# Performance work log

Hardware: AMD Instinct MI355X
Metric: run time of the kernel (lower is better)

The kernel has to match this reference:

```python
import jax, jax.numpy as jnp
import numpy as np

B, N_LEAVES, HID, NCLS, VOCAB = 32, 512, 128, 2, 50257
N_NODES = 2 * N_LEAVES - 1  # complete binary tree, heap layout


def setup_inputs() -> dict:
    key = jax.random.key(0)
    ks = jax.random.split(key, 12)
    x = jax.random.randint(ks[0], (B, N_NODES), 0, VOCAB)
    cue = jax.random.randint(ks[1], (B, N_NODES), 0, NCLS)
    # word j sits at tree leaf node L-1+j
    word_index = jnp.tile(jnp.arange(N_LEAVES - 1, 2 * N_LEAVES - 1), (B, 1))
    # parent->child adjacency stored in adj[:, 1]
    A = np.zeros((2, N_NODES, N_NODES), dtype=bool)
    p = np.arange(N_LEAVES - 1)
    A[1, p, 2 * p + 1] = True
    A[1, p, 2 * p + 2] = True
    adj = jnp.asarray(np.broadcast_to(A, (B, 2, N_NODES, N_NODES)).copy())
    s = 0.05
    emb = jax.random.normal(ks[2], (VOCAB, HID - NCLS)) * s
    Wc = jax.random.normal(ks[3], (HID, 2 * HID)) * s
    bc = jax.random.normal(ks[4], (HID,)) * s
    Wd = jax.random.normal(ks[5], (2 * HID, 2 * HID)) * s
    bd = jax.random.normal(ks[6], (2 * HID,)) * s
    Wg = jax.random.normal(ks[7], (HID, HID)) * s
    bg = jax.random.normal(ks[8], (HID,)) * s
    Wcl = jax.random.normal(ks[9], (NCLS, 2 * HID)) * s
    bcl = jax.random.normal(ks[10], (NCLS,)) * s
    return dict(x=x, word_index=word_index, cue=cue, adj=adj, emb=emb,
                Wc=Wc, bc=bc, Wd=Wd, bd=bd, Wg=Wg, bg=bg, Wcl=Wcl, bcl=bcl)


def reference(x, word_index, cue, adj, emb, Wc, bc, Wd, bd, Wg, bg, Wcl, bcl):
    # adj encodes the same complete binary heap tree that is hardcoded below
    Bn, N = x.shape
    H = Wc.shape[0]
    C = bcl.shape[0]
    L = (N + 1) // 2
    depth = L.bit_length() - 1  # leaves live at level `depth`
    bidx = jnp.arange(Bn)[:, None]

    word_emb = emb[x]                                   # (B, N, H-C)
    cue_oh = jax.nn.one_hot(cue, C, dtype=word_emb.dtype)
    in_feats = jnp.concatenate([word_emb, cue_oh], -1)  # (B, N, H)
    sent = in_feats[bidx, word_index]                   # (B, L, H) leaf feats

    # ---- upward compose: level-batched bottom-up traversal ----
    h = jnp.zeros((Bn, N, H), in_feats.dtype).at[bidx, word_index].set(sent)
    for d in range(depth - 1, -1, -1):
        p = jnp.arange(2 ** d - 1, 2 ** (d + 1) - 1)
        ctx = jnp.concatenate([h[:, 2 * p + 1], h[:, 2 * p + 2]], -1)  # (B, 2^d, 2H)
        h = h.at[:, p].set(jnp.tanh(ctx @ Wc.T + bc))
    # upward_results never writes leaf rows -> leaves stay zero
    up = h.at[bidx, word_index].set(0.0)

    g_down = jax.nn.sigmoid(h[:, 0] @ Wg.T + bg)        # (B, H)

    # ---- downward decompose: level-batched top-down traversal ----
    down = jnp.zeros_like(h).at[:, 0].set(g_down)
    for d in range(depth):
        p = jnp.arange(2 ** d - 1, 2 ** (d + 1) - 1)
        ctx = jnp.concatenate([down[:, p], up[:, p]], -1)
        ch = jnp.tanh(ctx @ Wd.T + bd)                  # (B, 2^d, 2H)
        down = down.at[:, 2 * p + 1].set(ch[..., :H]).at[:, 2 * p + 2].set(ch[..., H:])

    tree = jnp.concatenate([down, up], -1)              # (B, N, 2H)
    scores = jax.nn.sigmoid(tree @ Wcl.T + bcl)
    return jax.nn.softmax(scores, -1)
```

## Files before the change

### kernel.cpp

```cpp
#include <hip/hip_runtime.h>
#include <hip/hip_fp16.h>


constexpr int NNODES = 1023;

typedef _Float16 h2 __attribute__((ext_vector_type(2)));

__device__ __forceinline__ float dot2(uint a, uint b, float c) {
  union { uint u; h2 h; } x, y;
  x.u = a; y.u = b;
  return __builtin_amdgcn_fdot2(x.h, y.h, c, false);
}

__device__ __forceinline__ uint f2h2(float a, float b) {
  return (uint)__half_as_ushort(__float2half_rn(a)) |
         ((uint)__half_as_ushort(__float2half_rn(b)) << 16);
}

__device__ __forceinline__ float2 h2f2(uint u) {
  union { uint u; h2 h; } c; c.u = u;
  return make_float2((float)c.h.x, (float)c.h.y);
}

__device__ __forceinline__ void load_wslice(const float* __restrict__ Wrow,
                                            int l16, int m, uint* wout) {
  const float4 f0 = *(const float4*)(Wrow + l16 * 8 + m * 128);
  const float4 f1 = *(const float4*)(Wrow + l16 * 8 + m * 128 + 4);
  wout[0] = f2h2(f0.x, f0.y);
  wout[1] = f2h2(f0.z, f0.w);
  wout[2] = f2h2(f1.x, f1.y);
  wout[3] = f2h2(f1.z, f1.w);
}

__device__ __forceinline__ float fold16(const float* a, int l) {
  float b[8];
#pragma unroll
  for (int u = 0; u < 8; ++u) {
    const float mine = (l & 1) ? a[2 * u + 1] : a[2 * u];
    const float oth  = (l & 1) ? a[2 * u]     : a[2 * u + 1];
    b[u] = mine + __shfl_xor(oth, 1);
  }
  float c[4];
#pragma unroll
  for (int u = 0; u < 4; ++u) {
    const float mine = (l & 2) ? b[2 * u + 1] : b[2 * u];
    const float oth  = (l & 2) ? b[2 * u]     : b[2 * u + 1];
    c[u] = mine + __shfl_xor(oth, 2);
  }
  float d[2];
#pragma unroll
  for (int u = 0; u < 2; ++u) {
    const float mine = (l & 4) ? c[2 * u + 1] : c[2 * u];
    const float oth  = (l & 4) ? c[2 * u]     : c[2 * u + 1];
    d[u] = mine + __shfl_xor(oth, 4);
  }
  const float mine = (l & 8) ? d[1] : d[0];
  const float oth  = (l & 8) ? d[0] : d[1];
  return mine + __shfl_xor(oth, 8);
}

__device__ __forceinline__ float fold8(const float* a, int l) {
  float b[4];
#pragma unroll
  for (int u = 0; u < 4; ++u) {
    const float mine = (l & 1) ? a[2 * u + 1] : a[2 * u];
    const float oth  = (l & 1) ? a[2 * u]     : a[2 * u + 1];
    b[u] = mine + __shfl_xor(oth, 1);
  }
  float c[2];
#pragma unroll
  for (int u = 0; u < 2; ++u) {
    const float mine = (l & 2) ? b[2 * u + 1] : b[2 * u];
    const float oth  = (l & 2) ? b[2 * u]     : b[2 * u + 1];
    c[u] = mine + __shfl_xor(oth, 2);
  }
  const float mine = (l & 4) ? c[1] : c[0];
  const float oth  = (l & 4) ? c[0] : c[1];
  return mine + __shfl_xor(oth, 4);
}

__device__ __forceinline__ float fold4(const float* a, int l) {
  float b[2];
#pragma unroll
  for (int u = 0; u < 2; ++u) {
    const float mine = (l & 1) ? a[2 * u + 1] : a[2 * u];
    const float oth  = (l & 1) ? a[2 * u]     : a[2 * u + 1];
    b[u] = mine + __shfl_xor(oth, 1);
  }
  const float mine = (l & 2) ? b[1] : b[0];
  const float oth  = (l & 2) ? b[0] : b[1];
  return mine + __shfl_xor(oth, 2);
}

template<int CH>
__device__ __forceinline__ float foldCH(const float (&a)[CH * 4], int l16) {
  if constexpr (CH == 4) {
    return fold16(a, l16);
  } else if constexpr (CH == 2) {
    float t = fold8(a, l16);
    t += __shfl_xor(t, 8);
    return t;
  } else {
    float t = fold4(a, l16);
    t += __shfl_xor(t, 4);
    t += __shfl_xor(t, 8);
    return t;
  }
}

template<int CH>
__device__ __forceinline__ void up_pass(uint* __restrict__ heap2, int base, int cb,
                                        int cbase, const uint (&w)[4][8],
                                        float bias_r, int g, int l16, bool wr) {
  float a[CH * 4];
#pragma unroll
  for (int v = 0; v < CH * 4; ++v) a[v] = 0.f;
#pragma unroll
  for (int p = 0; p < CH; ++p) {
    const uint* cp = heap2 + (cb + 2 * (cbase + p)) * 64 + l16 * 4;
#pragma unroll
    for (int m = 0; m < 2; ++m) {
      const uint4 cc = *(const uint4*)(cp + m * 64);
#pragma unroll
      for (int r = 0; r < 4; ++r) {
        float av = a[p * 4 + r];
        av = dot2(w[r][m * 4 + 0], cc.x, av);
        av = dot2(w[r][m * 4 + 1], cc.y, av);
        av = dot2(w[r][m * 4 + 2], cc.z, av);
        av = dot2(w[r][m * 4 + 3], cc.w, av);
        a[p * 4 + r] = av;
      }
    }
  }
  const float tot = foldCH<CH>(a, l16);
  if (wr && l16 < CH * 4) {
    _Float16* hH = (_Float16*)heap2;
    hH[(base + cbase + (l16 >> 2)) * 128 + 4 * g + (l16 & 3)] =
        (_Float16)tanhf(tot + bias_r);
  }
}

template<int NP, int NH>
__device__ __forceinline__ void up_level16(uint* __restrict__ heap2,
                                           const uint (&w)[4][8],
                                           float bias_r, int g, int l16, int ph) {
  constexpr int base = NP - 1, cb = 2 * NP - 1;
  if constexpr (NP >= 4 * NH) {
#pragma unroll
    for (int c0 = 0; c0 < NP; c0 += 4 * NH)
      up_pass<4>(heap2, base, cb, c0 + ph * 4, w, bias_r, g, l16, true);
  } else if constexpr (NP * 2 == 4 * NH) {
    up_pass<2>(heap2, base, cb, ph * 2, w, bias_r, g, l16, true);
  } else if constexpr (NP == NH) {
    up_pass<1>(heap2, base, cb, ph, w, bias_r, g, l16, true);
  } else {
    up_pass<1>(heap2, base, cb, 0, w, bias_r, g, l16, ph == 0);
  }
  __syncthreads();
}

template<int CH>
__device__ __forceinline__ void down_pass(uint* __restrict__ db2,
                                          const uint* __restrict__ ub2,
                                          int base, int cb, int cbase,
                                          const uint (&w)[4][8],
                                          float bias_r, int g, int l16) {
  float a[CH * 4];
#pragma unroll
  for (int v = 0; v < CH * 4; ++v) a[v] = 0.f;
#pragma unroll
  for (int p = 0; p < CH; ++p) {
    const uint* dp = db2 + (base + cbase + p) * 64 + l16 * 4;
    const uint* up = ub2 + (base + cbase + p) * 64 + l16 * 4;
    const uint4 c0 = *(const uint4*)dp;
    const uint4 c1 = *(const uint4*)up;
#pragma unroll
    for (int r = 0; r < 4; ++r) {
      float av = a[p * 4 + r];
      av = dot2(w[r][0], c0.x, av);
      av = dot2(w[r][1], c0.y, av);
      av = dot2(w[r][2], c0.z, av);
      av = dot2(w[r][3], c0.w, av);
      av = dot2(w[r][4], c1.x, av);
      av = dot2(w[r][5], c1.y, av);
      av = dot2(w[r][6], c1.z, av);
      av = dot2(w[r][7], c1.w, av);
      a[p * 4 + r] = av;
    }
  }
  const float tot = foldCH<CH>(a, l16);
  if (l16 < CH * 4) {
    const int row = 4 * g + (l16 & 3);
    ((_Float16*)db2)[(cb + 2 * (cbase + (l16 >> 2)) + (row >> 7)) * 128 + (row & 127)] =
        (_Float16)tanhf(tot + bias_r);
  }
}

template<int NP>
__device__ __forceinline__ void down_level16(uint* __restrict__ db2,
                                             const uint* __restrict__ ub2,
                                             const uint (&w)[4][8],
                                             float bias_r, int g, int l16) {
  constexpr int base = NP - 1, cb = 2 * NP - 1;
  if constexpr (NP >= 4) {
#pragma unroll
    for (int c0 = 0; c0 < NP; c0 += 4)
      down_pass<4>(db2, ub2, base, cb, c0, w, bias_r, g, l16);
  } else {
    down_pass<NP>(db2, ub2, base, cb, 0, w, bias_r, g, l16);
  }
  __syncthreads();
}

template<int NP>
__device__ __forceinline__ void down_level16_dual(uint* __restrict__ A0,
                                                  const uint* __restrict__ B0,
                                                  uint* __restrict__ A1,
                                                  const uint* __restrict__ B1,
                                                  const uint (&w)[4][8],
                                                  float bias_r, int g, int l16) {
  constexpr int base = NP - 1, cb = 2 * NP - 1;
  if constexpr (NP >= 4) {
#pragma unroll
    for (int c0 = 0; c0 < NP; c0 += 4) {
      down_pass<4>(A0, B0, base, cb, c0, w, bias_r, g, l16);
      down_pass<4>(A1, B1, base, cb, c0, w, bias_r, g, l16);
    }
  } else {
    down_pass<NP>(A0, B0, base, cb, 0, w, bias_r, g, l16);
    down_pass<NP>(A1, B1, base, cb, 0, w, bias_r, g, l16);
  }
  __syncthreads();
}

__device__ __forceinline__ void classify16(const uint* __restrict__ dn2,
                                           const uint* __restrict__ un2,
                                           const float* __restrict__ wcl,
                                           const float* __restrict__ bcl,
                                           float* __restrict__ o, int l16) {
  const int k0 = l16 * 8;
  float s0 = 0.f, s1 = 0.f;
  {
    const uint4 du = *(const uint4*)(dn2 + l16 * 4);
    const float2 d0 = h2f2(du.x), d1 = h2f2(du.y), d2 = h2f2(du.z), d3 = h2f2(du.w);
    s0 += d0.x * wcl[k0]     + d0.y * wcl[k0 + 1] + d1.x * wcl[k0 + 2] + d1.y * wcl[k0 + 3]
        + d2.x * wcl[k0 + 4] + d2.y * wcl[k0 + 5] + d3.x * wcl[k0 + 6] + d3.y * wcl[k0 + 7];
    s1 += d0.x * wcl[256 + k0]     + d0.y * wcl[256 + k0 + 1]
        + d1.x * wcl[256 + k0 + 2] + d1.y * wcl[256 + k0 + 3]
        + d2.x * wcl[256 + k0 + 4] + d2.y * wcl[256 + k0 + 5]
        + d3.x * wcl[256 + k0 + 6] + d3.y * wcl[256 + k0 + 7];
  }
  if (un2) {
    const uint4 uu = *(const uint4*)(un2 + l16 * 4);
    const float2 u0 = h2f2(uu.x), u1 = h2f2(uu.y), u2 = h2f2(uu.z), u3 = h2f2(uu.w);
    s0 += u0.x * wcl[128 + k0]     + u0.y * wcl[128 + k0 + 1]
        + u1.x * wcl[128 + k0 + 2] + u1.y * wcl[128 + k0 + 3]
        + u2.x * wcl[128 + k0 + 4] + u2.y * wcl[128 + k0 + 5]
        + u3.x * wcl[128 + k0 + 6] + u3.y * wcl[128 + k0 + 7];
    s1 += u0.x * wcl[384 + k0]     + u0.y * wcl[384 + k0 + 1]
        + u1.x * wcl[384 + k0 + 2] + u1.y * wcl[384 + k0 + 3]
        + u2.x * wcl[384 + k0 + 4] + u2.y * wcl[384 + k0 + 5]
        + u3.x * wcl[384 + k0 + 6] + u3.y * wcl[384 + k0 + 7];
  }
#pragma unroll
  for (int m = 8; m >= 1; m >>= 1) {
    s0 += __shfl_xor(s0, m);
    s1 += __shfl_xor(s1, m);
  }
  if (l16 == 0) {
    s0 += bcl[0]; s1 += bcl[1];
    const float p0 = 1.f / (1.f + expf(-s0));
    const float p1 = 1.f / (1.f + expf(-s1));
    const float mx = fmaxf(p0, p1);
    const float e0 = expf(p0 - mx), e1 = expf(p1 - mx);
    const float inv = 1.f / (e0 + e1);
    o[0] = e0 * inv;
    o[1] = e1 * inv;
  }
}

__global__ __launch_bounds__(512, 4) void kA_up(const int* __restrict__ x,
                                                const int* __restrict__ cue,
                                                const float* __restrict__ emb,
                                                const float* __restrict__ Wc,
                                                const float* __restrict__ bc,
                                                uint* __restrict__ hw) {
  __shared__ __align__(16) uint heap2[63 * 64];
  __shared__ __align__(16) uint pad[10240];
  const int b = blockIdx.x >> 4, s = blockIdx.x & 15, r = 15 + s;
  const int t = threadIdx.x, g = t >> 4, l16 = t & 15;
  if (t == 0) ((volatile uint*)pad)[0] = 0u;

  uint w[4][8];
#pragma unroll
  for (int rr = 0; rr < 4; ++rr)
#pragma unroll
    for (int m = 0; m < 2; ++m)
      load_wslice(Wc + (4 * g + rr) * 256, l16, m, &w[rr][m * 4]);
  const float bias_r = bc[4 * g + (l16 & 3)];

  for (int idx = t; idx < 32 * 64; idx += 512) {
    const int j = idx >> 6, c = idx & 63, k0 = 2 * c;
    const int gq = ((r + 1) << 5) - 1 + j;
    const int xi = x[b * NNODES + gq], ci = cue[b * NNODES + gq];
    const float v0 = (k0 < 126) ? emb[(long long)xi * 126 + k0]
                                : ((ci == (k0 - 126)) ? 1.f : 0.f);
    const float v1 = (k0 + 1 < 126) ? emb[(long long)xi * 126 + k0 + 1]
                                    : ((ci == (k0 + 1 - 126)) ? 1.f : 0.f);
    heap2[(31 + j) * 64 + c] = f2h2(v0, v1);
  }
  __syncthreads();

  up_level16<16, 1>(heap2, w, bias_r, g, l16, 0);
  up_level16<8, 1>(heap2, w, bias_r, g, l16, 0);
  up_level16<4, 1>(heap2, w, bias_r, g, l16, 0);
  up_level16<2, 1>(heap2, w, bias_r, g, l16, 0);
  up_level16<1, 1>(heap2, w, bias_r, g, l16, 0);

  uint4* dst = (uint4*)(hw + (size_t)(b * 16 + s) * 31 * 64);
  const uint4* src = (const uint4*)heap2;
  for (int idx = t; idx < 31 * 16; idx += 512) dst[idx] = src[idx];
}

__global__ __launch_bounds__(1024, 4) void kC_all(const float* __restrict__ Wc,
                                                  const float* __restrict__ bc,
                                                  const float* __restrict__ Wg,
                                                  const float* __restrict__ bg,
                                                  const float* __restrict__ Wd,
                                                  const float* __restrict__ bd,
                                                  const float* __restrict__ Wcl,
                                                  const float* __restrict__ bcl,
                                                  const uint* __restrict__ hw,
                                                  float* __restrict__ out) {
  __shared__ __align__(16) uint A2[2 * 63 * 64];
  __shared__ __align__(16) uint B2[2 * 31 * 64];
  __shared__ __align__(16) uint rootdn2[128];
  __shared__ __align__(16) float wcl[512];
  __shared__ __align__(16) uint pad[8192];
  const int b = blockIdx.x >> 3, sp = blockIdx.x & 7;
  const int t = threadIdx.x, g = t >> 4, l16 = t & 15;
  if (t == 0) ((volatile uint*)pad)[0] = 0u;
  uint* A1 = A2 + 63 * 64;
  uint* B1 = B2 + 31 * 64;

  for (int idx = t; idx < 16 * 16; idx += 1024) {
    const int s = idx >> 4, q = idx & 15;
    *((uint4*)(B2 + (15 + s) * 64) + q) =
        *((const uint4*)(hw + (size_t)(b * 16 + s) * 31 * 64) + q);
  }
  if (t < 512) wcl[t] = Wcl[t];
  __syncthreads();

  {
    const int gu = g & 31, ph = t >> 9;
    uint wu[4][8];
#pragma unroll
    for (int rr = 0; rr < 4; ++rr)
#pragma unroll
      for (int m = 0; m < 2; ++m)
        load_wslice(Wc + (4 * gu + rr) * 256, l16, m, &wu[rr][m * 4]);
    const float bias_u = bc[4 * gu + (l16 & 3)];
    up_level16<8, 2>(B2, wu, bias_u, gu, l16, ph);
    up_level16<4, 2>(B2, wu, bias_u, gu, l16, ph);
    up_level16<2, 2>(B2, wu, bias_u, gu, l16, ph);
    up_level16<1, 2>(B2, wu, bias_u, gu, l16, ph);

    uint wg[4][4];
#pragma unroll
    for (int rr = 0; rr < 4; ++rr)
      load_wslice(Wg + (4 * gu + rr) * 128, l16, 0, &wg[rr][0]);
    float a[4];
#pragma unroll
    for (int v = 0; v < 4; ++v) a[v] = 0.f;
    {
      const uint4 cc = *(const uint4*)(B2 + l16 * 4);
#pragma unroll
      for (int rr = 0; rr < 4; ++rr) {
        float av = a[rr];
        av = dot2(wg[rr][0], cc.x, av);
        av = dot2(wg[rr][1], cc.y, av);
        av = dot2(wg[rr][2], cc.z, av);
        av = dot2(wg[rr][3], cc.w, av);
        a[rr] = av;
      }
    }
    float tot = fold4(a, l16);
    tot += __shfl_xor(tot, 4);
    tot += __shfl_xor(tot, 8);
    if (ph == 0 && l16 < 4) {
      const int row = 4 * gu + l16;
      ((_Float16*)A2)[row] = (_Float16)(1.f / (1.f + expf(-(tot + bg[row]))));
    }
    __syncthreads();
  }
  asm volatile("" ::: "memory");

  uint w[4][8];
#pragma unroll
  for (int rr = 0; rr < 4; ++rr)
#pragma unroll
    for (int m = 0; m < 2; ++m)
      load_wslice(Wd + (4 * g + rr) * 256, l16, m, &w[rr][m * 4]);
  const float bias_r = bd[4 * g + (l16 & 3)];

  down_level16<1>(A2, B2, w, bias_r, g, l16);
  down_level16<2>(A2, B2, w, bias_r, g, l16);
  down_level16<4>(A2, B2, w, bias_r, g, l16);
  down_level16<8>(A2, B2, w, bias_r, g, l16);

  if (sp == 0 && t < 15 * 16) {
    const int m = t >> 4;
    classify16(A2 + m * 64, B2 + m * 64, wcl, bcl,
               out + ((size_t)b * NNODES + m) * 2, l16);
  }
  if (t < 128) rootdn2[t] = A2[(15 + sp * 2 + (t >> 6)) * 64 + (t & 63)];
  __syncthreads();

  for (int idx = t; idx < 2 * 31 * 16; idx += 1024) {
    const int ss = (idx >= 31 * 16) ? 1 : 0;
    const int k4 = idx - ss * 31 * 16;
    ((uint4*)(B2 + ss * 31 * 64))[k4] =
        ((const uint4*)(hw + (size_t)(b * 16 + sp * 2 + ss) * 31 * 64))[k4];
  }
  if (t < 128) A2[(t >> 6) * 63 * 64 + (t & 63)] = rootdn2[t];
  __syncthreads();

  down_level16_dual<1>(A2, B2, A1, B1, w, bias_r, g, l16);
  down_level16_dual<2>(A2, B2, A1, B1, w, bias_r, g, l16);
  down_level16_dual<4>(A2, B2, A1, B1, w, bias_r, g, l16);
  down_level16_dual<8>(A2, B2, A1, B1, w, bias_r, g, l16);
  down_level16_dual<16>(A2, B2, A1, B1, w, bias_r, g, l16);

  if (t < 63 * 16) {
    const int m = t >> 4;
    const int lvl = 31 - __clz(m + 1);
    const int j = (m + 1) - (1 << lvl);
#pragma unroll
    for (int ss = 0; ss < 2; ++ss) {
      const int r = 15 + sp * 2 + ss;
      const int gq = ((r + 1) << lvl) - 1 + j;
      classify16(A2 + ss * 63 * 64 + m * 64,
                 (m < 31) ? (B2 + ss * 31 * 64 + m * 64) : nullptr, wcl, bcl,
                 out + ((size_t)b * NNODES + gq) * 2, l16);
    }
  }
}

extern "C" void kernel_launch(void* const* d_in, const int* in_sizes, int n_in,
                              void* d_out, int out_size, void* d_ws, size_t ws_size,
                              hipStream_t stream) {
  const int*   x   = (const int*)d_in[0];
  const int*   cue = (const int*)d_in[2];
  const float* emb = (const float*)d_in[4];
  const float* Wc  = (const float*)d_in[5];
  const float* bc  = (const float*)d_in[6];
  const float* Wd  = (const float*)d_in[7];
  const float* bd  = (const float*)d_in[8];
  const float* Wg  = (const float*)d_in[9];
  const float* bg  = (const float*)d_in[10];
  const float* Wcl = (const float*)d_in[11];
  const float* bcl = (const float*)d_in[12];
  float* out = (float*)d_out;

  uint* hw = (uint*)d_ws;

  hipLaunchKernelGGL(kA_up,  dim3(512), dim3(512), 0, stream, x, cue, emb, Wc, bc, hw);
  hipLaunchKernelGGL(kC_all, dim3(256), dim3(1024), 0, stream,
                     Wc, bc, Wg, bg, Wd, bd, Wcl, bcl, hw, out);
}
```

Baseline: 70.38 us.

## Split final downward levels across two half-blocks, each computing both child halves

The final downward phase used to have all 1024 threads process both subtrees back to back, each thread owning 4 output rows of Wd. Now each 512-thread half of the block handles one subtree, and each thread holds weights for 8 rows (both the left-child and right-child halves), so a single pair of context loads feeds twice as many dot products. This halves the LDS reads of context per output and removes the serial pairing of subtrees. The cost is double the weight registers per thread (64 uints), which may pressure occupancy under the 1024-thread launch bounds. The upward helpers are renamed and specialised with no change in behaviour.

Result: slower. 75.54 us (+7.3%).

```diff
diff --git a/kernel.cpp b/kernel.cpp
--- a/kernel.cpp
+++ b/kernel.cpp
@@ -134,24 +134,38 @@
   }
   const float tot = foldCH<CH>(a, l16);
   if (wr && l16 < CH * 4) {
-    _Float16* hH = (_Float16*)heap2;
-    hH[(base + cbase + (l16 >> 2)) * 128 + 4 * g + (l16 & 3)] =
+    ((_Float16*)heap2)[(base + cbase + (l16 >> 2)) * 128 + 4 * g + (l16 & 3)] =
         (_Float16)tanhf(tot + bias_r);
   }
 }
 
-template<int NP, int NH>
-__device__ __forceinline__ void up_level16(uint* __restrict__ heap2,
-                                           const uint (&w)[4][8],
-                                           float bias_r, int g, int l16, int ph) {
+template<int NP>
+__device__ __forceinline__ void up_level512(uint* __restrict__ heap2,
+                                            const uint (&w)[4][8],
+                                            float bias_r, int g, int l16) {
   constexpr int base = NP - 1, cb = 2 * NP - 1;
-  if constexpr (NP >= 4 * NH) {
-#pragma unroll
-    for (int c0 = 0; c0 < NP; c0 += 4 * NH)
+  if constexpr (NP >= 4) {
+#pragma unroll
+    for (int c0 = 0; c0 < NP; c0 += 4)
+      up_pass<4>(heap2, base, cb, c0, w, bias_r, g, l16, true);
+  } else {
+    up_pass<NP>(heap2, base, cb, 0, w, bias_r, g, l16, true);
+  }
+  __syncthreads();
+}
+
+template<int NP>
+__device__ __forceinline__ void up_level16x2(uint* __restrict__ heap2,
+                                             const uint (&w)[4][8],
+                                             float bias_r, int g, int l16, int ph) {
+  constexpr int base = NP - 1, cb = 2 * NP - 1;
+  if constexpr (NP >= 8) {
+#pragma unroll
+    for (int c0 = 0; c0 < NP; c0 += 8)
       up_pass<4>(heap2, base, cb, c0 + ph * 4, w, bias_r, g, l16, true);
-  } else if constexpr (NP * 2 == 4 * NH) {
+  } else if constexpr (NP == 4) {
     up_pass<2>(heap2, base, cb, ph * 2, w, bias_r, g, l16, true);
-  } else if constexpr (NP == NH) {
+  } else if constexpr (NP == 2) {
     up_pass<1>(heap2, base, cb, ph, w, bias_r, g, l16, true);
   } else {
     up_pass<1>(heap2, base, cb, 0, w, bias_r, g, l16, ph == 0);
@@ -170,10 +184,8 @@
   for (int v = 0; v < CH * 4; ++v) a[v] = 0.f;
 #pragma unroll
   for (int p = 0; p < CH; ++p) {
-    const uint* dp = db2 + (base + cbase + p) * 64 + l16 * 4;
-    const uint* up = ub2 + (base + cbase + p) * 64 + l16 * 4;
-    const uint4 c0 = *(const uint4*)dp;
-    const uint4 c1 = *(const uint4*)up;
+    const uint4 c0 = *(const uint4*)(db2 + (base + cbase + p) * 64 + l16 * 4);
+    const uint4 c1 = *(const uint4*)(ub2 + (base + cbase + p) * 64 + l16 * 4);
 #pragma unroll
     for (int r = 0; r < 4; ++r) {
       float av = a[p * 4 + r];
@@ -212,23 +224,67 @@
   __syncthreads();
 }
 
+template<int CH>
+__device__ __forceinline__ void down_pass8(uint* __restrict__ db2,
+                                           const uint* __restrict__ ub2,
+                                           int base, int cb, int cbase,
+                                           const uint (&w)[2][4][8],
+                                           float bias0, float bias1,
+                                           int g, int l16) {
+  float a0[CH * 4], a1[CH * 4];
+#pragma unroll
+  for (int v = 0; v < CH * 4; ++v) { a0[v] = 0.f; a1[v] = 0.f; }
+#pragma unroll
+  for (int p = 0; p < CH; ++p) {
+    const uint4 c0 = *(const uint4*)(db2 + (base + cbase + p) * 64 + l16 * 4);
+    const uint4 c1 = *(const uint4*)(ub2 + (base + cbase + p) * 64 + l16 * 4);
+#pragma unroll
+    for (int r = 0; r < 4; ++r) {
+      float av = a0[p * 4 + r];
+      av = dot2(w[0][r][0], c0.x, av);
+      av = dot2(w[0][r][1], c0.y, av);
+      av = dot2(w[0][r][2], c0.z, av);
+      av = dot2(w[0][r][3], c0.w, av);
+      av = dot2(w[0][r][4], c1.x, av);
+      av = dot2(w[0][r][5], c1.y, av);
+      av = dot2(w[0][r][6], c1.z, av);
+      av = dot2(w[0][r][7], c1.w, av);
+      a0[p * 4 + r] = av;
+      float bv = a1[p * 4 + r];
+      bv = dot2(w[1][r][0], c0.x, bv);
+      bv = dot2(w[1][r][1], c0.y, bv);
+      bv = dot2(w[1][r][2], c0.z, bv);
+      bv = dot2(w[1][r][3], c0.w, bv);
+      bv = dot2(w[1][r][4], c1.x, bv);
+      bv = dot2(w[1][r][5], c1.y, bv);
+      bv = dot2(w[1][r][6], c1.z, bv);
+      bv = dot2(w[1][r][7], c1.w, bv);
+      a1[p * 4 + r] = bv;
+    }
+  }
+  const float t0 = foldCH<CH>(a0, l16);
+  const float t1 = foldCH<CH>(a1, l16);
+  if (l16 < CH * 4) {
+    const int p = l16 >> 2, col = 4 * g + (l16 & 3);
+    _Float16* dH = (_Float16*)db2;
+    dH[(cb + 2 * (cbase + p)) * 128 + col]     = (_Float16)tanhf(t0 + bias0);
+    dH[(cb + 2 * (cbase + p) + 1) * 128 + col] = (_Float16)tanhf(t1 + bias1);
+  }
+}
+
 template<int NP>
-__device__ __forceinline__ void down_level16_dual(uint* __restrict__ A0,
-                                                  const uint* __restrict__ B0,
-                                                  uint* __restrict__ A1,
-                                                  const uint* __restrict__ B1,
-                                                  const uint (&w)[4][8],
-                                                  float bias_r, int g, int l16) {
+__device__ __forceinline__ void down_level8_half(uint* __restrict__ db2,
+                                                 const uint* __restrict__ ub2,
+                                                 const uint (&w)[2][4][8],
+                                                 float bias0, float bias1,
+                                                 int g, int l16) {
   constexpr int base = NP - 1, cb = 2 * NP - 1;
   if constexpr (NP >= 4) {
 #pragma unroll
-    for (int c0 = 0; c0 < NP; c0 += 4) {
-      down_pass<4>(A0, B0, base, cb, c0, w, bias_r, g, l16);
-      down_pass<4>(A1, B1, base, cb, c0, w, bias_r, g, l16);
-    }
+    for (int c0 = 0; c0 < NP; c0 += 4)
+      down_pass8<4>(db2, ub2, base, cb, c0, w, bias0, bias1, g, l16);
   } else {
-    down_pass<NP>(A0, B0, base, cb, 0, w, bias_r, g, l16);
-    down_pass<NP>(A1, B1, base, cb, 0, w, bias_r, g, l16);
+    down_pass8<NP>(db2, ub2, base, cb, 0, w, bias0, bias1, g, l16);
   }
   __syncthreads();
 }
@@ -311,11 +367,11 @@
   }
   __syncthreads();
 
-  up_level16<16, 1>(heap2, w, bias_r, g, l16, 0);
-  up_level16<8, 1>(heap2, w, bias_r, g, l16, 0);
-  up_level16<4, 1>(heap2, w, bias_r, g, l16, 0);
-  up_level16<2, 1>(heap2, w, bias_r, g, l16, 0);
-  up_level16<1, 1>(heap2, w, bias_r, g, l16, 0);
+  up_level512<16>(heap2, w, bias_r, g, l16);
+  up_level512<8>(heap2, w, bias_r, g, l16);
+  up_level512<4>(heap2, w, bias_r, g, l16);
+  up_level512<2>(heap2, w, bias_r, g, l16);
+  up_level512<1>(heap2, w, bias_r, g, l16);
 
   uint4* dst = (uint4*)(hw + (size_t)(b * 16 + s) * 31 * 64);
   const uint4* src = (const uint4*)heap2;
@@ -340,8 +396,6 @@
   const int b = blockIdx.x >> 3, sp = blockIdx.x & 7;
   const int t = threadIdx.x, g = t >> 4, l16 = t & 15;
   if (t == 0) ((volatile uint*)pad)[0] = 0u;
-  uint* A1 = A2 + 63 * 64;
-  uint* B1 = B2 + 31 * 64;
 
   for (int idx = t; idx < 16 * 16; idx += 1024) {
     const int s = idx >> 4, q = idx & 15;
@@ -360,10 +414,10 @@
       for (int m = 0; m < 2; ++m)
         load_wslice(Wc + (4 * gu + rr) * 256, l16, m, &wu[rr][m * 4]);
     const float bias_u = bc[4 * gu + (l16 & 3)];
-    up_level16<8, 2>(B2, wu, bias_u, gu, l16, ph);
-    up_level16<4, 2>(B2, wu, bias_u, gu, l16, ph);
-    up_level16<2, 2>(B2, wu, bias_u, gu, l16, ph);
-    up_level16<1, 2>(B2, wu, bias_u, gu, l16, ph);
+    up_level16x2<8>(B2, wu, bias_u, gu, l16, ph);
+    up_level16x2<4>(B2, wu, bias_u, gu, l16, ph);
+    up_level16x2<2>(B2, wu, bias_u, gu, l16, ph);
+    up_level16x2<1>(B2, wu, bias_u, gu, l16, ph);
 
     uint wg[4][4];
 #pragma unroll
@@ -395,18 +449,19 @@
   }
   asm volatile("" ::: "memory");
 
-  uint w[4][8];
-#pragma unroll
-  for (int rr = 0; rr < 4; ++rr)
-#pragma unroll
-    for (int m = 0; m < 2; ++m)
-      load_wslice(Wd + (4 * g + rr) * 256, l16, m, &w[rr][m * 4]);
-  const float bias_r = bd[4 * g + (l16 & 3)];
-
-  down_level16<1>(A2, B2, w, bias_r, g, l16);
-  down_level16<2>(A2, B2, w, bias_r, g, l16);
-  down_level16<4>(A2, B2, w, bias_r, g, l16);
-  down_level16<8>(A2, B2, w, bias_r, g, l16);
+  {
+    uint w[4][8];
+#pragma unroll
+    for (int rr = 0; rr < 4; ++rr)
+#pragma unroll
+      for (int m = 0; m < 2; ++m)
+        load_wslice(Wd + (4 * g + rr) * 256, l16, m, &w[rr][m * 4]);
+    const float bias_r = bd[4 * g + (l16 & 3)];
+    down_level16<1>(A2, B2, w, bias_r, g, l16);
+    down_level16<2>(A2, B2, w, bias_r, g, l16);
+    down_level16<4>(A2, B2, w, bias_r, g, l16);
+    down_level16<8>(A2, B2, w, bias_r, g, l16);
+  }
 
   if (sp == 0 && t < 15 * 16) {
     const int m = t >> 4;
@@ -425,11 +480,27 @@
   if (t < 128) A2[(t >> 6) * 63 * 64 + (t & 63)] = rootdn2[t];
   __syncthreads();
 
-  down_level16_dual<1>(A2, B2, A1, B1, w, bias_r, g, l16);
-  down_level16_dual<2>(A2, B2, A1, B1, w, bias_r, g, l16);
-  down_level16_dual<4>(A2, B2, A1, B1, w, bias_r, g, l16);
-  down_level16_dual<8>(A2, B2, A1, B1, w, bias_r, g, l16);
-  down_level16_dual<16>(A2, B2, A1, B1, w, bias_r, g, l16);
+  {
+    const int h = t >> 9, tt = t & 511, gs = tt >> 4;
+    uint* As = A2 + h * 63 * 64;
+    uint* Bs = B2 + h * 31 * 64;
+    uint w8[2][4][8];
+#pragma unroll
+    for (int h2 = 0; h2 < 2; ++h2)
+#pragma unroll
+      for (int rr = 0; rr < 4; ++rr)
+#pragma unroll
+        for (int m = 0; m < 2; ++m)
+          load_wslice(Wd + (h2 * 128 + 4 * gs + rr) * 256, l16, m, &w8[h2][rr][m * 4]);
+    const float bias0 = bd[4 * gs + (l16 & 3)];
+    const float bias1 = bd[128 + 4 * gs + (l16 & 3)];
+
+    down_level8_half<1>(As, Bs, w8, bias0, bias1, gs, l16);
+    down_level8_half<2>(As, Bs, w8, bias0, bias1, gs, l16);
+    down_level8_half<4>(As, Bs, w8, bias0, bias1, gs, l16);
+    down_level8_half<8>(As, Bs, w8, bias0, bias1, gs, l16);
+    down_level8_half<16>(As, Bs, w8, bias0, bias1, gs, l16);
+  }
 
   if (t < 63 * 16) {
     const int m = t >> 4;
```
